# Optimization experiments

Hardware: AMD Instinct MI355X
Metric: run time of the kernel (lower is better)

Reference implementation:

```python
import jax, jax.numpy as jnp
import numpy as np

# Lorentz (hyperboloid) manifold, curvature parameter K: x0 = sqrt(K + ||x_space||^2)
K = 1.0
LN_EPS = 1e-5
PROJ_EPS = 1e-6
L, D, H, B, S, V = 12, 512, 8, 2, 1024, 50257
DH = D // H  # 64 space dims per head


def add_time(space):
    # lift space components onto the hyperboloid
    t = jnp.sqrt(jnp.sum(space * space, axis=-1, keepdims=True) + K)
    return jnp.concatenate([t, space], axis=-1)


def l_project(z):
    # renormalize an ambient vector onto the hyperboloid (Lorentz midpoint / LResNet normalization)
    inner = -jnp.square(z[..., :1]) + jnp.sum(jnp.square(z[..., 1:]), axis=-1, keepdims=True)
    return jnp.sqrt(K) * z / jnp.sqrt(jnp.clip(-inner, PROJ_EPS, None))


def l_layernorm(x, g, b):
    # LayerNorm on the space part, recompute time
    s = x[..., 1:]
    mu = jnp.mean(s, axis=-1, keepdims=True)
    var = jnp.var(s, axis=-1, keepdims=True)
    s = (s - mu) * jax.lax.rsqrt(var + LN_EPS) * g + b
    return add_time(s)


def setup_inputs() -> dict:
    key = jax.random.key(0)
    ks = jax.random.split(key, 12)
    std_in = D ** -0.5
    std_out = (2 * D * L) ** -0.5  # out_proj_std from the torch init
    inp = {}
    inp['text_tokens'] = jax.random.randint(ks[0], (B, S), 0, V)
    inp['embed_table'] = jax.random.normal(ks[1], (V, D - 1), jnp.float32) * 0.02
    inp['Wq'] = jax.random.normal(ks[2], (L, D, D), jnp.float32) * std_in
    inp['bq'] = jnp.zeros((L, D), jnp.float32)
    inp['Wk'] = jax.random.normal(ks[3], (L, D, D), jnp.float32) * std_in
    inp['bk'] = jnp.zeros((L, D), jnp.float32)
    inp['Wv'] = jax.random.normal(ks[4], (L, D, D), jnp.float32) * std_in
    inp['bv'] = jnp.zeros((L, D), jnp.float32)
    inp['Wo'] = jax.random.normal(ks[5], (L, H * (DH + 1), D - 1), jnp.float32) * std_in
    inp['bo'] = jnp.zeros((L, D - 1), jnp.float32)
    inp['ln1_g'] = jnp.ones((L, D - 1), jnp.float32)
    inp['ln1_b'] = jnp.zeros((L, D - 1), jnp.float32)
    inp['ln2_g'] = jnp.ones((L, D - 1), jnp.float32)
    inp['ln2_b'] = jnp.zeros((L, D - 1), jnp.float32)
    inp['Wfc'] = jax.random.normal(ks[6], (L, D, 4 * D - 1), jnp.float32) * std_in
    inp['bfc'] = jnp.zeros((L, 4 * D - 1), jnp.float32)
    inp['Wpr'] = jax.random.normal(ks[7], (L, 4 * D, D - 1), jnp.float32) * std_out
    inp['bpr'] = jnp.zeros((L, D - 1), jnp.float32)
    inp['res_w1'] = jnp.ones((L,), jnp.float32)
    inp['res_w2'] = jnp.ones((L,), jnp.float32)
    inp['Wfin'] = jax.random.normal(ks[8], (D, D - 1), jnp.float32) * std_in
    inp['bfin'] = jnp.zeros((D - 1,), jnp.float32)
    inp['lnf_g'] = jnp.ones((D - 1,), jnp.float32)
    inp['lnf_b'] = jnp.zeros((D - 1,), jnp.float32)
    return inp


def reference(text_tokens, embed_table, Wq, bq, Wk, bk, Wv, bv, Wo, bo, ln1_g, ln1_b,
              ln2_g, ln2_b, Wfc, bfc, Wpr, bpr, res_w1, res_w2, Wfin, bfin, lnf_g, lnf_b):
    b, s = text_tokens.shape
    scale = 1.0 / np.sqrt(DH)
    # LorentzEmbeddings: space-part lookup, time recomputed
    x = add_time(embed_table[text_tokens])  # [B, S, D]
    causal = jnp.tril(jnp.ones((s, s), bool))  # True = attend
    for i in range(L):
        # --- Lorentz multi-head self-attention ---
        lx = l_layernorm(x, ln1_g[i], ln1_b[i])
        q = add_time((lx @ Wq[i] + bq[i]).reshape(b, s, H, DH))  # [B,S,H,DH+1]
        k = add_time((lx @ Wk[i] + bk[i]).reshape(b, s, H, DH))
        v = add_time((lx @ Wv[i] + bv[i]).reshape(b, s, H, DH))
        qm = jnp.concatenate([-q[..., :1], q[..., 1:]], axis=-1)  # apply Minkowski metric
        linner = jnp.einsum('bihd,bjhd->bhij', qm, k)  # Lorentz inner product <q_i, k_j>_L
        scores = (2.0 * K + 2.0 * linner) * scale     # = -d_L^2(q,k)/sqrt(dh)
        scores = jnp.where(causal[None, None], scores, -1e9)
        a = jax.nn.softmax(scores, axis=-1)
        agg = jnp.einsum('bhij,bjhd->bihd', a, v)      # Lorentz centroid numerator
        agg = l_project(agg)                           # normalize back to hyperboloid
        ax = add_time(agg.reshape(b, s, H * (DH + 1)) @ Wo[i] + bo[i])  # heads-concat proj
        x = l_project(x + res_w1[i] * ax)              # LResNet residual 1
        # --- Lorentz MLP ---
        h = l_layernorm(x, ln2_g[i], ln2_b[i])
        h = add_time(h @ Wfc[i] + bfc[i])              # c_fc: D -> 4D ambient
        h = add_time(jax.nn.gelu(h[..., 1:]))          # LorentzActivation (GELU on space)
        h = add_time(h @ Wpr[i] + bpr[i])              # c_proj: 4D -> D ambient
        x = l_project(x + res_w2[i] * h)               # LResNet residual 2
    x = add_time(x @ Wfin + bfin)                      # final_proj
    x = l_layernorm(x, lnf_g, lnf_b)                   # ln_final
    return x
```

## Files before the change

### kernel.cpp

```cpp
#include <hip/hip_runtime.h>
#include <cstdint>

typedef _Float16 f16;
typedef _Float16 f16x8 __attribute__((ext_vector_type(8)));
typedef float f32x4 __attribute__((ext_vector_type(4)));
typedef unsigned int u32;

#define DEV __device__ __forceinline__

DEV void gll16(const void* g, void* l) {
  __builtin_amdgcn_global_load_lds((const __attribute__((address_space(1))) u32*)g,
                                   (__attribute__((address_space(3))) u32*)l, 16, 0, 0);
}

DEV float block_sum(float v, float* red) {
#pragma unroll
  for (int o = 32; o; o >>= 1) v += __shfl_xor(v, o);
  int w = threadIdx.x >> 6;
  __syncthreads();
  if ((threadIdx.x & 63) == 0) red[w] = v;
  __syncthreads();
  return red[0] + red[1] + red[2] + red[3];
}

__global__ void k_trans(const float* __restrict__ W0, f16* __restrict__ BT0, int K, int N, int Kpad,
                        size_t srcStride, size_t dstStride) {
  __shared__ float t[32][33];
  const float* W = W0 + (size_t)blockIdx.z * srcStride;
  f16* BT = BT0 + (size_t)blockIdx.z * dstStride;
  int n0 = blockIdx.x * 32, k0 = blockIdx.y * 32, tx = threadIdx.x, ty = threadIdx.y;
  for (int i = ty; i < 32; i += 8) {
    int k = k0 + i, n = n0 + tx;
    t[i][tx] = (k < K && n < N) ? W[(size_t)k * N + n] : 0.f;
  }
  __syncthreads();
  for (int i = ty; i < 32; i += 8)
    BT[(size_t)(n0 + i) * Kpad + k0 + tx] = (f16)t[tx][i];
}

__global__ void k_trans3(const float* __restrict__ Wq, const float* __restrict__ Wk,
                         const float* __restrict__ Wv, f16* __restrict__ BT) {
  __shared__ float t[32][33];
  const int layer = blockIdx.z / 3, typ = blockIdx.z % 3;
  const float* W = ((typ == 0) ? Wq : (typ == 1) ? Wk : Wv) + (size_t)layer * 262144;
  f16* dst = BT + (size_t)layer * 786432 + (size_t)typ * 262144;
  int n0 = blockIdx.x * 32, k0 = blockIdx.y * 32, tx = threadIdx.x, ty = threadIdx.y;
  for (int i = ty; i < 32; i += 8) t[i][tx] = W[(size_t)(k0 + i) * 512 + n0 + tx];
  __syncthreads();
  for (int i = ty; i < 32; i += 8) dst[(size_t)(n0 + i) * 512 + k0 + tx] = (f16)t[tx][i];
}

template <int BM, int BN, int KZ, int EPI>
__global__ __launch_bounds__((BM == 128) ? 512 : 256)
void k_gemm(const f16* __restrict__ A, const f16* __restrict__ B,
            int lda, int ldb, int klen, int GM,
            float* __restrict__ O1, float* __restrict__ O2,
            float* __restrict__ O3, float* __restrict__ O4, int ldc,
            const float* __restrict__ c0, const float* __restrict__ c1,
            const float* __restrict__ c2, float* __restrict__ ssq,
            f16* __restrict__ H1, f16* __restrict__ H2, f16* __restrict__ H3) {
  constexpr int NW = (BM == 128) ? 8 : 4;
  constexpr int WM = (BM == 128) ? 4 : 2;
  constexpr int FN = BN / ((NW / WM) * 16);
  const int tid = threadIdx.x, wid = tid >> 6, lane = tid & 63;
  const int l15 = lane & 15, l4 = lane >> 4;
  const int wm = wid % WM, wn = wid / WM;
  const int nwg = gridDim.x;
  int lin = blockIdx.x;
  int wg = (lin & 7) * (nwg >> 3) + (lin >> 3);
  int tn = wg / (GM * KZ);
  int rem = wg - tn * (GM * KZ);
  int tm = rem / KZ, tz = rem - (rem / KZ) * KZ;
  const int m0 = tm * BM, n0 = tn * BN, kbeg = tz * klen, ksteps = klen / 64;
  __shared__ __align__(16) char SM[(BM + BN) * 256];
  f32x4 acc[2][FN];
#pragma unroll
  for (int i = 0; i < 2; i++)
#pragma unroll
    for (int j = 0; j < FN; j++) acc[i][j] = (f32x4){0.f, 0.f, 0.f, 0.f};
  const size_t ldab = (size_t)lda * 2, ldbb = (size_t)ldb * 2;
  const int swz = ((lane & 7) ^ (lane >> 3)) * 16;
  const char* Ab = (const char*)A + (size_t)(m0 + (lane >> 3)) * ldab + swz + (size_t)kbeg * 2;
  const char* Bb = (const char*)B + (size_t)(n0 + (lane >> 3)) * ldbb + swz + (size_t)kbeg * 2;
  auto stage = [&](int buf, int ks) {
    char* da = SM + buf * (BM * 128);
    char* db = SM + 2 * BM * 128 + buf * (BN * 128);
    for (int i = wid; i < BM / 8; i += NW)
      gll16(Ab + (size_t)(i * 8) * ldab + (size_t)ks * 128, da + i * 1024);
    for (int i = wid; i < BN / 8; i += NW)
      gll16(Bb + (size_t)(i * 8) * ldbb + (size_t)ks * 128, db + i * 1024);
  };
  stage(0, 0);
  asm volatile("s_waitcnt vmcnt(0)" ::: "memory");
  __builtin_amdgcn_s_barrier();
  __builtin_amdgcn_sched_barrier(0);
  int cur = 0;
  for (int ks = 0; ks < ksteps; ks++) {
    const bool more = (ks + 1 < ksteps);
    if (more) {
      stage(cur ^ 1, ks + 1);
      asm volatile("s_waitcnt vmcnt(4)" ::: "memory");
    } else {
      asm volatile("s_waitcnt vmcnt(0)" ::: "memory");
    }
    __builtin_amdgcn_s_barrier();
    __builtin_amdgcn_sched_barrier(0);
    const f16* sA = (const f16*)(SM + cur * (BM * 128));
    const f16* sB = (const f16*)(SM + 2 * BM * 128 + cur * (BN * 128));
#pragma unroll
    for (int kk = 0; kk < 2; kk++) {
      f16x8 af[2], bf[FN];
#pragma unroll
      for (int i = 0; i < 2; i++) {
        int row = wm * 32 + i * 16 + l15;
        af[i] = *(const f16x8*)(sA + row * 64 + (((kk * 4 + l4) ^ (l15 & 7)) * 8));
      }
#pragma unroll
      for (int j = 0; j < FN; j++) {
        int row = wn * (FN * 16) + j * 16 + l15;
        bf[j] = *(const f16x8*)(sB + row * 64 + (((kk * 4 + l4) ^ (l15 & 7)) * 8));
      }
#pragma unroll
      for (int i = 0; i < 2; i++)
#pragma unroll
        for (int j = 0; j < FN; j++)
          acc[i][j] = __builtin_amdgcn_mfma_f32_16x16x32_f16(af[i], bf[j], acc[i][j], 0, 0, 0);
    }
    __builtin_amdgcn_sched_barrier(0);
    __builtin_amdgcn_s_barrier();
    cur ^= 1;
  }
  if (EPI == 0) {
#pragma unroll
    for (int i = 0; i < 2; i++) {
      int row0 = m0 + wm * 32 + i * 16 + l4 * 4;
#pragma unroll
      for (int j = 0; j < FN; j++) {
        int col = n0 + wn * (FN * 16) + j * 16 + l15;
#pragma unroll
        for (int r = 0; r < 4; r++) O1[(size_t)(row0 + r) * ldc + col] = acc[i][j][r];
      }
    }
  } else if (EPI == 1) {
    const int cb = (n0 >> 6) + wn;
    const int typ = cb >> 3, h = cb & 7;
    const float* bb = (typ == 0) ? c0 : (typ == 1) ? c1 : c2;
    float bj[FN];
#pragma unroll
    for (int j = 0; j < FN; j++) bj[j] = bb[h * 64 + j * 16 + l15];
    const float qs = (typ == 0) ? 0.25f : 1.0f;
#pragma unroll
    for (int i = 0; i < 2; i++) {
#pragma unroll
      for (int r = 0; r < 4; r++) {
        float y[FN], ss = 0.f;
#pragma unroll
        for (int j = 0; j < FN; j++) { y[j] = acc[i][j][r] + bj[j]; ss += y[j] * y[j]; }
        ss += __shfl_xor(ss, 1); ss += __shfl_xor(ss, 2);
        ss += __shfl_xor(ss, 4); ss += __shfl_xor(ss, 8);
        float t = sqrtf(ss + 1.f);
        int row = m0 + wm * 32 + i * 16 + l4 * 4 + r;
        int b = row >> 10, s = row & 1023, bh = b * 8 + h;
        if (typ < 2) {
          f16* dst = typ ? H2 : H1;
          size_t base = ((size_t)bh * 1024 + s) * 88;
#pragma unroll
          for (int j = 0; j < FN; j++) dst[base + j * 16 + l15] = (f16)(qs * y[j]);
          if (l15 == 0) dst[base + 64] = (f16)(qs * t);
        } else {
#pragma unroll
          for (int j = 0; j < FN; j++)
            H3[((size_t)bh * 80 + j * 16 + l15) * 1024 + s] = (f16)y[j];
          if (l15 == 0) H3[((size_t)bh * 80 + 64) * 1024 + s] = (f16)t;
        }
      }
    }
  } else if (EPI == 2) {
#pragma unroll
    for (int i = 0; i < 2; i++) {
#pragma unroll
      for (int r = 0; r < 4; r++) {
        int row = m0 + wm * 32 + i * 16 + l4 * 4 + r;
        float ss = 0.f;
#pragma unroll
        for (int j = 0; j < FN; j++) {
          int col = n0 + wn * (FN * 16) + j * 16 + l15;
          float gg = 0.f;
          if (col < 2047) {
            float yv = acc[i][j][r] + c0[col];
            float cc = yv * yv * yv;
            gg = 0.5f * yv * (1.f + tanhf(0.7978845608f * (yv + 0.044715f * cc)));
          }
          ss += gg * gg;
          H1[(size_t)row * 2048 + col] = (f16)gg;
        }
        ss += __shfl_xor(ss, 1); ss += __shfl_xor(ss, 2);
        ss += __shfl_xor(ss, 4); ss += __shfl_xor(ss, 8);
        if (l15 == 0) atomicAdd(ssq + row, ss);
      }
    }
  } else {
    float* O = (tz == 0) ? O1 : (tz == 1) ? O2 : (tz == 2) ? O3 : O4;
#pragma unroll
    for (int i = 0; i < 2; i++) {
#pragma unroll
      for (int r = 0; r < 4; r++) {
        int row = m0 + wm * 32 + i * 16 + l4 * 4 + r;
        float t = 0.f;
        if (tz == 0) t = sqrtf(ssq[row] + 1.f);
#pragma unroll
        for (int j = 0; j < FN; j++) {
          int col = n0 + wn * (FN * 16) + j * 16 + l15;
          float v = acc[i][j][r];
          if (tz == 0) v += t * ((col < 511) ? c0[col] : 0.f);
          O[(size_t)row * ldc + col] = v;
        }
      }
    }
  }
}

__global__ void k_embed(const int* __restrict__ tok, const float* __restrict__ tbl,
                        const float* __restrict__ g, const float* __restrict__ bsh,
                        float* __restrict__ x, f16* __restrict__ act) {
  __shared__ float red[4];
  const int m = blockIdx.x, tid = threadIdx.x;
  const float* e = tbl + (size_t)tok[m] * 511;
  float e0 = (tid < 511) ? e[tid] : 0.f;
  float e1 = (tid + 256 < 511) ? e[tid + 256] : 0.f;
  float s1 = block_sum(e0 + e1, red);
  float s2 = block_sum(e0 * e0 + e1 * e1, red);
  float t = sqrtf(s2 + 1.f);
  float* xr = x + (size_t)m * 512;
  if (tid == 0) xr[0] = t;
  if (tid < 511) xr[1 + tid] = e0;
  if (tid + 256 < 511) xr[257 + tid] = e1;
  float mu = s1 / 511.f;
  float var = s2 / 511.f - mu * mu;
  float inv = rsqrtf(var + 1e-5f);
  float n0 = (tid < 511) ? (e0 - mu) * inv * g[tid] + bsh[tid] : 0.f;
  float n1 = (tid + 256 < 511) ? (e1 - mu) * inv * g[tid + 256] + bsh[tid + 256] : 0.f;
  float sn = block_sum(n0 * n0 + n1 * n1, red);
  float t2 = sqrtf(sn + 1.f);
  f16* ar = act + (size_t)m * 512;
  if (tid == 0) ar[0] = (f16)t2;
  if (tid < 511) ar[1 + tid] = (f16)n0;
  if (tid + 256 < 511) ar[257 + tid] = (f16)n1;
}

__launch_bounds__(64)
__global__ void k_attn(const f16* __restrict__ qhat, const f16* __restrict__ khat,
                       const f16* __restrict__ vT, f16* __restrict__ ao) {
  __shared__ f16 sP[16 * 88];
  const int lin = blockIdx.x;
  const int wg = (lin & 7) * 128 + (lin >> 3);
  const int bh = wg >> 6, rt = 63 - (wg & 63);
  const int lane = threadIdx.x, l15 = lane & 15, l4 = lane >> 4;
  const f16* qp = qhat + ((size_t)bh * 1024 + rt * 16) * 88;
  const f16* kp = khat + (size_t)bh * 1024 * 88;
  const f16* vp = vT + (size_t)bh * 80 * 1024;
  f16x8 qf0 = *(const f16x8*)(qp + l15 * 88 + l4 * 8);
  f16x8 qf1 = *(const f16x8*)(qp + l15 * 88 + 32 + l4 * 8);
  float qth[4];
#pragma unroll
  for (int r = 0; r < 4; r++) qth[r] = (float)qp[(l4 * 4 + r) * 88 + 64];
  f32x4 acc[5];
#pragma unroll
  for (int i = 0; i < 5; i++) acc[i] = (f32x4){0, 0, 0, 0};
  float mrun[4] = {-3e38f, -3e38f, -3e38f, -3e38f}, lrun[4] = {0, 0, 0, 0};
  const int nt = (rt >> 2) + 1;
  for (int jt = 0; jt < nt; ++jt) {
    const int j0 = jt * 64;
    const bool dt = (jt == nt - 1);
    f32x4 sc[4];
#pragma unroll
    for (int fn = 0; fn < 4; fn++) {
      const f16* kb = kp + (size_t)(j0 + fn * 16 + l15) * 88;
      f16x8 k0v = *(const f16x8*)(kb + l4 * 8);
      f16x8 k1v = *(const f16x8*)(kb + 32 + l4 * 8);
      f32x4 a = (f32x4){0, 0, 0, 0};
      a = __builtin_amdgcn_mfma_f32_16x16x32_f16(qf0, k0v, a, 0, 0, 0);
      a = __builtin_amdgcn_mfma_f32_16x16x32_f16(qf1, k1v, a, 0, 0, 0);
      sc[fn] = a;
    }
    float s[4][4];
#pragma unroll
    for (int fn = 0; fn < 4; fn++) {
      float ktc = (float)kp[(size_t)(j0 + fn * 16 + l15) * 88 + 64];
      int col = j0 + fn * 16 + l15;
#pragma unroll
      for (int r = 0; r < 4; r++) {
        int row = rt * 16 + l4 * 4 + r;
        float v = sc[fn][r] - qth[r] * ktc;
        s[fn][r] = (!dt || col <= row) ? v : -3e38f;
      }
    }
    float mnew[4], al[4], rs[4];
#pragma unroll
    for (int r = 0; r < 4; r++) {
      float t = fmaxf(fmaxf(s[0][r], s[1][r]), fmaxf(s[2][r], s[3][r]));
#pragma unroll
      for (int o = 8; o; o >>= 1) t = fmaxf(t, __shfl_xor(t, o));
      mnew[r] = fmaxf(mrun[r], t);
      al[r] = exp2f((mrun[r] - mnew[r]) * 1.44269504f);
      mrun[r] = mnew[r];
      rs[r] = 0.f;
    }
#pragma unroll
    for (int fn = 0; fn < 4; fn++)
#pragma unroll
      for (int r = 0; r < 4; r++) {
        float p = exp2f((s[fn][r] - mnew[r]) * 1.44269504f);
        rs[r] += p;
        sP[(l4 * 4 + r) * 88 + fn * 16 + l15] = (f16)p;
      }
#pragma unroll
    for (int r = 0; r < 4; r++) {
#pragma unroll
      for (int o = 8; o; o >>= 1) rs[r] += __shfl_xor(rs[r], o);
      lrun[r] = lrun[r] * al[r] + rs[r];
    }
#pragma unroll
    for (int fd = 0; fd < 5; fd++)
#pragma unroll
      for (int r = 0; r < 4; r++) acc[fd][r] *= al[r];
    asm volatile("s_waitcnt lgkmcnt(0)" ::: "memory");
    __builtin_amdgcn_sched_barrier(0);
#pragma unroll
    for (int ks = 0; ks < 2; ks++) {
      f16x8 pf = *(const f16x8*)(sP + l15 * 88 + ks * 32 + l4 * 8);
#pragma unroll
      for (int fd = 0; fd < 5; fd++) {
        f16x8 vf = *(const f16x8*)(vp + (size_t)(fd * 16 + l15) * 1024 + j0 + ks * 32 + l4 * 8);
        acc[fd] = __builtin_amdgcn_mfma_f32_16x16x32_f16(pf, vf, acc[fd], 0, 0, 0);
      }
    }
  }
  const int b = bh >> 3, h = bh & 7;
#pragma unroll
  for (int r = 0; r < 4; r++) {
    float invl = 1.0f / lrun[r];
    float ss = 0.f, ov[4];
#pragma unroll
    for (int fd = 0; fd < 4; fd++) { ov[fd] = acc[fd][r] * invl; ss += ov[fd] * ov[fd]; }
#pragma unroll
    for (int o = 8; o; o >>= 1) ss += __shfl_xor(ss, o);
    float tv = acc[4][r] * invl;
    tv = __shfl(tv, lane & 48);
    float scp = rsqrtf(fmaxf(tv * tv - ss, 1e-6f));
    int row = rt * 16 + l4 * 4 + r;
    size_t rowbase = ((size_t)b * 1024 + row) * 576;
    size_t rb = rowbase + h * 65;
    if (l15 == 0) ao[rb] = (f16)(tv * scp);
#pragma unroll
    for (int fd = 0; fd < 4; fd++) ao[rb + 1 + fd * 16 + l15] = (f16)(ov[fd] * scp);
    for (int c = l15; c < 56; c += 16) ao[rowbase + 520 + c] = (f16)0.f;
  }
}

__global__ void k_resproj(float* __restrict__ x, const float* __restrict__ r1,
                          const float* __restrict__ r2, const float* __restrict__ r3,
                          const float* __restrict__ r4, int np,
                          const float* __restrict__ bias, const float* __restrict__ resw, int li,
                          const float* __restrict__ g, const float* __restrict__ bsh,
                          f16* __restrict__ act, int applyLN, float* __restrict__ ssq) {
  __shared__ float red[4];
  const int m = blockIdx.x, tid = threadIdx.x;
  const size_t rb = (size_t)m * 512;
  float* xr = x + rb;
  const float rw = resw[li];
  if (tid == 0) ssq[m] = 0.f;
  float y0 = 0.f, y1 = 0.f;
  if (tid < 511) {
    y0 = r1[rb + tid];
    if (np == 4) y0 += r2[rb + tid] + r3[rb + tid] + r4[rb + tid];
    y0 += bias[tid];
  }
  if (tid + 256 < 511) {
    y1 = r1[rb + tid + 256];
    if (np == 4) y1 += r2[rb + tid + 256] + r3[rb + tid + 256] + r4[rb + tid + 256];
    y1 += bias[tid + 256];
  }
  float s2 = block_sum(y0 * y0 + y1 * y1, red);
  float tax = sqrtf(s2 + 1.f);
  float xt = xr[0];
  float u0 = (tid < 511) ? xr[1 + tid] + rw * y0 : 0.f;
  float u1 = (tid + 256 < 511) ? xr[257 + tid] + rw * y1 : 0.f;
  float ut = xt + rw * tax;
  float su = block_sum(u0 + u1, red);
  float su2 = block_sum(u0 * u0 + u1 * u1, red);
  float scp = rsqrtf(fmaxf(ut * ut - su2, 1e-6f));
  float nx0 = u0 * scp, nx1 = u1 * scp, nxt = ut * scp;
  if (tid == 0) xr[0] = nxt;
  if (tid < 511) xr[1 + tid] = nx0;
  if (tid + 256 < 511) xr[257 + tid] = nx1;
  f16* ar = act + rb;
  if (applyLN) {
    float mu = su * scp / 511.f;
    float var = su2 * scp * scp / 511.f - mu * mu;
    float inv = rsqrtf(var + 1e-5f);
    float n0 = (tid < 511) ? (nx0 - mu) * inv * g[tid] + bsh[tid] : 0.f;
    float n1 = (tid + 256 < 511) ? (nx1 - mu) * inv * g[tid + 256] + bsh[tid + 256] : 0.f;
    float sn = block_sum(n0 * n0 + n1 * n1, red);
    float t2 = sqrtf(sn + 1.f);
    if (tid == 0) ar[0] = (f16)t2;
    if (tid < 511) ar[1 + tid] = (f16)n0;
    if (tid + 256 < 511) ar[257 + tid] = (f16)n1;
  } else {
    if (tid == 0) ar[0] = (f16)nxt;
    if (tid < 511) ar[1 + tid] = (f16)nx0;
    if (tid + 256 < 511) ar[257 + tid] = (f16)nx1;
  }
}

__global__ void k_final(const float* __restrict__ raw, const float* __restrict__ bias,
                        const float* __restrict__ g, const float* __restrict__ bsh,
                        float* __restrict__ out) {
  __shared__ float red[4];
  const int m = blockIdx.x, tid = threadIdx.x;
  const float* rr = raw + (size_t)m * 512;
  float y0 = (tid < 511) ? rr[tid] + bias[tid] : 0.f;
  float y1 = (tid + 256 < 511) ? rr[tid + 256] + bias[tid + 256] : 0.f;
  float s1 = block_sum(y0 + y1, red);
  float s2 = block_sum(y0 * y0 + y1 * y1, red);
  float mu = s1 / 511.f;
  float var = s2 / 511.f - mu * mu;
  float inv = rsqrtf(var + 1e-5f);
  float n0 = (tid < 511) ? (y0 - mu) * inv * g[tid] + bsh[tid] : 0.f;
  float n1 = (tid + 256 < 511) ? (y1 - mu) * inv * g[tid + 256] + bsh[tid + 256] : 0.f;
  float sn = block_sum(n0 * n0 + n1 * n1, red);
  float t2 = sqrtf(sn + 1.f);
  float* orow = out + (size_t)m * 512;
  if (tid == 0) orow[0] = t2;
  if (tid < 511) orow[1 + tid] = n0;
  if (tid + 256 < 511) orow[257 + tid] = n1;
}

extern "C" void kernel_launch(void* const* d_in, const int* in_sizes, int n_in,
                              void* d_out, int out_size, void* d_ws, size_t ws_size,
                              hipStream_t stream) {
  (void)in_sizes; (void)n_in; (void)out_size; (void)ws_size;
  const int* tok = (const int*)d_in[0];
  const float* etab = (const float*)d_in[1];
  const float* Wq = (const float*)d_in[2];
  const float* bq = (const float*)d_in[3];
  const float* Wk = (const float*)d_in[4];
  const float* bk = (const float*)d_in[5];
  const float* Wv = (const float*)d_in[6];
  const float* bv = (const float*)d_in[7];
  const float* Wo = (const float*)d_in[8];
  const float* bo = (const float*)d_in[9];
  const float* ln1g = (const float*)d_in[10];
  const float* ln1b = (const float*)d_in[11];
  const float* ln2g = (const float*)d_in[12];
  const float* ln2b = (const float*)d_in[13];
  const float* Wfc = (const float*)d_in[14];
  const float* bfc = (const float*)d_in[15];
  const float* Wpr = (const float*)d_in[16];
  const float* bpr = (const float*)d_in[17];
  const float* rw1 = (const float*)d_in[18];
  const float* rw2 = (const float*)d_in[19];
  const float* Wfin = (const float*)d_in[20];
  const float* bfin = (const float*)d_in[21];
  const float* lnfg = (const float*)d_in[22];
  const float* lnfb = (const float*)d_in[23];

  char* wsb = (char*)d_ws;
  size_t off = 0;
  auto alloc = [&](size_t bytes) -> char* {
    char* p = wsb + off;
    off = (off + bytes + 1023) & ~(size_t)1023;
    return p;
  };
  float* x = (float*)alloc(2048ull * 512 * 4);
  f16* actA = (f16*)alloc(2048ull * 512 * 2);
  float* raw1 = (float*)alloc(2048ull * 512 * 4);
  float* raw2 = (float*)alloc(2048ull * 512 * 4);
  float* raw3 = (float*)alloc(2048ull * 512 * 4);
  float* raw4 = (float*)alloc(2048ull * 512 * 4);
  float* ssq = (float*)alloc(2048ull * 4);
  f16* qhat = (f16*)alloc(16ull * 1024 * 88 * 2);
  f16* khat = (f16*)alloc(16ull * 1024 * 88 * 2);
  f16* vT = (f16*)alloc(16ull * 80 * 1024 * 2);
  f16* ao = (f16*)alloc(2048ull * 576 * 2);
  f16* fcact = (f16*)alloc(2048ull * 2048 * 2);
  f16* wqkvT = (f16*)alloc(12ull * 1536 * 512 * 2);
  f16* woT = (f16*)alloc(12ull * 512 * 576 * 2);
  f16* wfcT = (f16*)alloc(12ull * 2048 * 512 * 2);
  f16* wprT = (f16*)alloc(12ull * 512 * 2048 * 2);
  f16* wfinT = (f16*)alloc(512ull * 512 * 2);

  k_trans3<<<dim3(16, 16, 36), dim3(32, 8), 0, stream>>>(Wq, Wk, Wv, wqkvT);
  k_trans<<<dim3(16, 18, 12), dim3(32, 8), 0, stream>>>(Wo, woT, 520, 511, 576,
                                                        520ull * 511, 512ull * 576);
  k_trans<<<dim3(64, 16, 12), dim3(32, 8), 0, stream>>>(Wfc, wfcT, 512, 2047, 512,
                                                        512ull * 2047, 2048ull * 512);
  k_trans<<<dim3(16, 64, 12), dim3(32, 8), 0, stream>>>(Wpr + 511, wprT, 2047, 511, 2048,
                                                        2048ull * 511, 512ull * 2048);
  k_trans<<<dim3(16, 16, 1), dim3(32, 8), 0, stream>>>(Wfin, wfinT, 512, 511, 512, 0, 0);

  k_embed<<<2048, 256, 0, stream>>>(tok, etab, ln1g, ln1b, x, actA);

  for (int li = 0; li < 12; li++) {
    const f16* wqkvT_l = wqkvT + (size_t)li * 1536 * 512;
    const f16* woT_l = woT + (size_t)li * 512 * 576;
    const f16* wfcT_l = wfcT + (size_t)li * 2048 * 512;
    const f16* wprT_l = wprT + (size_t)li * 512 * 2048;
    const float* Wpr_l = Wpr + (size_t)li * 2048 * 511;
    const float* bq_l = bq + (size_t)li * 512;
    const float* bk_l = bk + (size_t)li * 512;
    const float* bv_l = bv + (size_t)li * 512;
    const float* bo_l = bo + (size_t)li * 511;
    const float* bfc_l = bfc + (size_t)li * 2047;
    const float* bpr_l = bpr + (size_t)li * 511;
    const float* ln2g_l = ln2g + (size_t)li * 511;
    const float* ln2b_l = ln2b + (size_t)li * 511;

    k_gemm<128, 128, 1, 1><<<192, 512, 0, stream>>>(
        actA, wqkvT_l, 512, 512, 512, 16, nullptr, nullptr, nullptr, nullptr, 0,
        bq_l, bk_l, bv_l, nullptr, qhat, khat, vT);
    k_attn<<<1024, 64, 0, stream>>>(qhat, khat, vT, ao);
    k_gemm<64, 64, 1, 0><<<256, 256, 0, stream>>>(
        ao, woT_l, 576, 576, 576, 32, raw1, nullptr, nullptr, nullptr, 512,
        nullptr, nullptr, nullptr, nullptr, nullptr, nullptr, nullptr);
    k_resproj<<<2048, 256, 0, stream>>>(x, raw1, raw1, raw1, raw1, 1, bo_l, rw1, li,
                                        ln2g_l, ln2b_l, actA, 1, ssq);
    k_gemm<128, 128, 1, 2><<<256, 512, 0, stream>>>(
        actA, wfcT_l, 512, 512, 512, 16, nullptr, nullptr, nullptr, nullptr, 0,
        bfc_l, nullptr, nullptr, ssq, fcact, nullptr, nullptr);
    k_gemm<64, 64, 4, 3><<<1024, 256, 0, stream>>>(
        fcact, wprT_l, 2048, 2048, 512, 32, raw1, raw2, raw3, raw4, 512,
        Wpr_l, nullptr, nullptr, ssq, nullptr, nullptr, nullptr);
    const float* ng = (li < 11) ? ln1g + (size_t)(li + 1) * 511 : ln1g;
    const float* nb = (li < 11) ? ln1b + (size_t)(li + 1) * 511 : ln1b;
    k_resproj<<<2048, 256, 0, stream>>>(x, raw1, raw2, raw3, raw4, 4, bpr_l, rw2, li,
                                        ng, nb, actA, (li < 11) ? 1 : 0, ssq);
  }

  k_gemm<64, 64, 1, 0><<<256, 256, 0, stream>>>(
      actA, wfinT, 512, 512, 512, 32, raw1, nullptr, nullptr, nullptr, 512,
      nullptr, nullptr, nullptr, nullptr, nullptr, nullptr, nullptr);
  k_final<<<2048, 256, 0, stream>>>(raw1, bfin, lnfg, lnfb, (float*)d_out);
}
```

Baseline: 1.630 ms.

## Fuse residual/LN row kernels into GEMM tails via last-arriver counters; merge prolog kernels

Removes the separate k_resproj and k_final launches. Each GEMM workgroup stores its partial tile with cache-bypassing stores and bumps a per-row-block atomic counter, and the last workgroup for a row block does the split-K reduction, residual projection and LayerNorm for that block. The weight transposes, embedding and counter reset are merged into one prolog launch. This saves launch overhead and a round trip of the row data, but the serial tail now runs on a single workgroup per row block.

```diff
diff --git a/kernel.cpp b/kernel.cpp
--- a/kernel.cpp
+++ b/kernel.cpp
@@ -12,42 +12,135 @@
   __builtin_amdgcn_global_load_lds((const __attribute__((address_space(1))) u32*)g,
                                    (__attribute__((address_space(3))) u32*)l, 16, 0, 0);
 }
-
-DEV float block_sum(float v, float* red) {
+DEV f32x4 ld16c(const void* p) {
+  f32x4 r;
+  asm volatile("global_load_dwordx4 %0, %1, off sc0 sc1" : "=&v"(r) : "v"(p) : "memory");
+  return r;
+}
+DEV float ld4p(const void* p) {
+  float r;
+  asm volatile("global_load_dword %0, %1, off" : "=&v"(r) : "v"(p) : "memory");
+  return r;
+}
+DEV void st4c(void* p, float v) {
+  asm volatile("global_store_dword %0, %1, off sc0 sc1" :: "v"(p), "v"(v) : "memory");
+}
+DEV void vmwait() {
+  asm volatile("s_waitcnt vmcnt(0)" ::: "memory");
+  __builtin_amdgcn_sched_barrier(0);
+}
+DEV u32 inc_rlx(u32* p) { return __hip_atomic_fetch_add(p, 1u, __ATOMIC_RELAXED, __HIP_MEMORY_SCOPE_AGENT); }
+
+DEV float wsum(float v) {
 #pragma unroll
   for (int o = 32; o; o >>= 1) v += __shfl_xor(v, o);
-  int w = threadIdx.x >> 6;
-  __syncthreads();
-  if ((threadIdx.x & 63) == 0) red[w] = v;
-  __syncthreads();
-  return red[0] + red[1] + red[2] + red[3];
-}
-
-__global__ void k_trans(const float* __restrict__ W0, f16* __restrict__ BT0, int K, int N, int Kpad,
-                        size_t srcStride, size_t dstStride) {
-  __shared__ float t[32][33];
-  const float* W = W0 + (size_t)blockIdx.z * srcStride;
-  f16* BT = BT0 + (size_t)blockIdx.z * dstStride;
-  int n0 = blockIdx.x * 32, k0 = blockIdx.y * 32, tx = threadIdx.x, ty = threadIdx.y;
-  for (int i = ty; i < 32; i += 8) {
-    int k = k0 + i, n = n0 + tx;
-    t[i][tx] = (k < K && n < N) ? W[(size_t)k * N + n] : 0.f;
-  }
-  __syncthreads();
-  for (int i = ty; i < 32; i += 8)
-    BT[(size_t)(n0 + i) * Kpad + k0 + tx] = (f16)t[tx][i];
-}
-
-__global__ void k_trans3(const float* __restrict__ Wq, const float* __restrict__ Wk,
-                         const float* __restrict__ Wv, f16* __restrict__ BT) {
-  __shared__ float t[32][33];
-  const int layer = blockIdx.z / 3, typ = blockIdx.z % 3;
-  const float* W = ((typ == 0) ? Wq : (typ == 1) ? Wk : Wv) + (size_t)layer * 262144;
-  f16* dst = BT + (size_t)layer * 786432 + (size_t)typ * 262144;
-  int n0 = blockIdx.x * 32, k0 = blockIdx.y * 32, tx = threadIdx.x, ty = threadIdx.y;
-  for (int i = ty; i < 32; i += 8) t[i][tx] = W[(size_t)(k0 + i) * 512 + n0 + tx];
-  __syncthreads();
-  for (int i = ty; i < 32; i += 8) dst[(size_t)(n0 + i) * 512 + k0 + tx] = (f16)t[tx][i];
+  return v;
+}
+
+template <int NP, int MODE>
+DEV void reduce_tile(int m0, const float* r1, const float* r2, const float* r3, const float* r4,
+                     const float* bias, float rw, const float* g, const float* bsh,
+                     float* x, f16* act, float* outp, float* ssqz, int applyLN) {
+  const int wid = threadIdx.x >> 6, lane = threadIdx.x & 63, cbase = lane * 8;
+  for (int t = 0; t < 16; t++) {
+    const int row = m0 + wid * 16 + t;
+    const size_t rb = (size_t)row * 512 + cbase;
+    f32x4 a0 = ld16c(r1 + rb), a1 = ld16c(r1 + rb + 4);
+    f32x4 b0, b1, c0v, c1v, d0, d1;
+    if (NP == 4) {
+      b0 = ld16c(r2 + rb); b1 = ld16c(r2 + rb + 4);
+      c0v = ld16c(r3 + rb); c1v = ld16c(r3 + rb + 4);
+      d0 = ld16c(r4 + rb); d1 = ld16c(r4 + rb + 4);
+    }
+    float xs[8]; float xt = 0.f;
+    if (MODE == 0) {
+      const float* xrowp = x + (size_t)row * 512;
+#pragma unroll
+      for (int j = 0; j < 8; j++) {
+        int c = cbase + j;
+        xs[j] = (c < 511) ? ld4p(xrowp + 1 + c) : 0.f;
+      }
+      xt = ld4p(xrowp);
+    }
+    vmwait();
+    float y[8];
+#pragma unroll
+    for (int j = 0; j < 4; j++) {
+      y[j] = a0[j]; y[4 + j] = a1[j];
+      if (NP == 4) { y[j] += b0[j] + c0v[j] + d0[j]; y[4 + j] += b1[j] + c1v[j] + d1[j]; }
+    }
+    float lss = 0.f;
+#pragma unroll
+    for (int j = 0; j < 8; j++) {
+      int c = cbase + j;
+      y[j] = (c < 511) ? (y[j] + bias[c]) : 0.f;
+      lss += y[j] * y[j];
+    }
+    float ss = wsum(lss);
+    if (MODE == 1) {
+      float lsu = 0.f;
+#pragma unroll
+      for (int j = 0; j < 8; j++) lsu += y[j];
+      float su = wsum(lsu);
+      float mu = su * (1.f / 511.f);
+      float var = ss * (1.f / 511.f) - mu * mu;
+      float inv = rsqrtf(var + 1e-5f);
+      float n[8], lsn = 0.f;
+#pragma unroll
+      for (int j = 0; j < 8; j++) {
+        int c = cbase + j;
+        n[j] = (c < 511) ? ((y[j] - mu) * inv * g[c] + bsh[c]) : 0.f;
+        lsn += n[j] * n[j];
+      }
+      float t2 = sqrtf(wsum(lsn) + 1.f);
+      float* orow = outp + (size_t)row * 512;
+      if (lane == 0) orow[0] = t2;
+#pragma unroll
+      for (int j = 0; j < 8; j++) { int c = cbase + j; if (c < 511) orow[1 + c] = n[j]; }
+    } else {
+      float tax = sqrtf(ss + 1.f);
+      float u[8], lsu = 0.f, lsu2 = 0.f;
+#pragma unroll
+      for (int j = 0; j < 8; j++) {
+        int c = cbase + j;
+        u[j] = (c < 511) ? (xs[j] + rw * y[j]) : 0.f;
+        lsu += u[j]; lsu2 += u[j] * u[j];
+      }
+      float su = wsum(lsu), su2 = wsum(lsu2);
+      float ut = xt + rw * tax;
+      float scp = rsqrtf(fmaxf(ut * ut - su2, 1e-6f));
+      float nxt = ut * scp;
+      float nx[8];
+#pragma unroll
+      for (int j = 0; j < 8; j++) nx[j] = u[j] * scp;
+      float* xrow = x + (size_t)row * 512;
+      if (lane == 0) xrow[0] = nxt;
+#pragma unroll
+      for (int j = 0; j < 8; j++) { int c = cbase + j; if (c < 511) xrow[1 + c] = nx[j]; }
+      if (NP == 4 && lane == 0) ssqz[row] = 0.f;
+      f16* arow = act + (size_t)row * 512;
+      if (applyLN) {
+        float mu = su * scp * (1.f / 511.f);
+        float var = su2 * scp * scp * (1.f / 511.f) - mu * mu;
+        float inv = rsqrtf(var + 1e-5f);
+        float n[8], lsn = 0.f;
+#pragma unroll
+        for (int j = 0; j < 8; j++) {
+          int c = cbase + j;
+          n[j] = (c < 511) ? ((nx[j] - mu) * inv * g[c] + bsh[c]) : 0.f;
+          lsn += n[j] * n[j];
+        }
+        float t2 = sqrtf(wsum(lsn) + 1.f);
+        if (lane == 0) arow[0] = (f16)t2;
+#pragma unroll
+        for (int j = 0; j < 8; j++) { int c = cbase + j; if (c < 511) arow[1 + c] = (f16)n[j]; }
+      } else {
+        if (lane == 0) arow[0] = (f16)nxt;
+#pragma unroll
+        for (int j = 0; j < 8; j++) { int c = cbase + j; if (c < 511) arow[1 + c] = (f16)nx[j]; }
+      }
+    }
+  }
 }
 
 template <int BM, int BN, int KZ, int EPI>
@@ -58,7 +151,10 @@
             float* __restrict__ O3, float* __restrict__ O4, int ldc,
             const float* __restrict__ c0, const float* __restrict__ c1,
             const float* __restrict__ c2, float* __restrict__ ssq,
-            f16* __restrict__ H1, f16* __restrict__ H2, f16* __restrict__ H3) {
+            f16* __restrict__ H1, f16* __restrict__ H2, f16* __restrict__ H3,
+            float* __restrict__ x, f16* __restrict__ act, float* __restrict__ outp,
+            const float* __restrict__ lng, const float* __restrict__ lnb,
+            const float* __restrict__ rwv, int li, int applyLN, u32* __restrict__ cnt) {
   constexpr int NW = (BM == 128) ? 8 : 4;
   constexpr int WM = (BM == 128) ? 4 : 2;
   constexpr int FN = BN / ((NW / WM) * 16);
@@ -73,6 +169,7 @@
   int tm = rem / KZ, tz = rem - (rem / KZ) * KZ;
   const int m0 = tm * BM, n0 = tn * BN, kbeg = tz * klen, ksteps = klen / 64;
   __shared__ __align__(16) char SM[(BM + BN) * 256];
+  __shared__ int sred;
   f32x4 acc[2][FN];
 #pragma unroll
   for (int i = 0; i < 2; i++)
@@ -130,18 +227,7 @@
     __builtin_amdgcn_s_barrier();
     cur ^= 1;
   }
-  if (EPI == 0) {
-#pragma unroll
-    for (int i = 0; i < 2; i++) {
-      int row0 = m0 + wm * 32 + i * 16 + l4 * 4;
-#pragma unroll
-      for (int j = 0; j < FN; j++) {
-        int col = n0 + wn * (FN * 16) + j * 16 + l15;
-#pragma unroll
-        for (int r = 0; r < 4; r++) O1[(size_t)(row0 + r) * ldc + col] = acc[i][j][r];
-      }
-    }
-  } else if (EPI == 1) {
+  if (EPI == 1) {
     const int cb = (n0 >> 6) + wn;
     const int typ = cb >> 3, h = cb & 7;
     const float* bb = (typ == 0) ? c0 : (typ == 1) ? c1 : c2;
@@ -175,6 +261,7 @@
         }
       }
     }
+    return;
   } else if (EPI == 2) {
 #pragma unroll
     for (int i = 0; i < 2; i++) {
@@ -199,7 +286,8 @@
         if (l15 == 0) atomicAdd(ssq + row, ss);
       }
     }
-  } else {
+    return;
+  } else if (EPI == 3) {
     float* O = (tz == 0) ? O1 : (tz == 1) ? O2 : (tz == 2) ? O3 : O4;
 #pragma unroll
     for (int i = 0; i < 2; i++) {
@@ -213,39 +301,124 @@
           int col = n0 + wn * (FN * 16) + j * 16 + l15;
           float v = acc[i][j][r];
           if (tz == 0) v += t * ((col < 511) ? c0[col] : 0.f);
-          O[(size_t)row * ldc + col] = v;
+          st4c(&O[(size_t)row * ldc + col], v);
         }
       }
     }
-  }
-}
-
-__global__ void k_embed(const int* __restrict__ tok, const float* __restrict__ tbl,
-                        const float* __restrict__ g, const float* __restrict__ bsh,
-                        float* __restrict__ x, f16* __restrict__ act) {
-  __shared__ float red[4];
-  const int m = blockIdx.x, tid = threadIdx.x;
-  const float* e = tbl + (size_t)tok[m] * 511;
-  float e0 = (tid < 511) ? e[tid] : 0.f;
-  float e1 = (tid + 256 < 511) ? e[tid + 256] : 0.f;
-  float s1 = block_sum(e0 + e1, red);
-  float s2 = block_sum(e0 * e0 + e1 * e1, red);
-  float t = sqrtf(s2 + 1.f);
-  float* xr = x + (size_t)m * 512;
-  if (tid == 0) xr[0] = t;
-  if (tid < 511) xr[1 + tid] = e0;
-  if (tid + 256 < 511) xr[257 + tid] = e1;
-  float mu = s1 / 511.f;
-  float var = s2 / 511.f - mu * mu;
-  float inv = rsqrtf(var + 1e-5f);
-  float n0 = (tid < 511) ? (e0 - mu) * inv * g[tid] + bsh[tid] : 0.f;
-  float n1 = (tid + 256 < 511) ? (e1 - mu) * inv * g[tid + 256] + bsh[tid + 256] : 0.f;
-  float sn = block_sum(n0 * n0 + n1 * n1, red);
-  float t2 = sqrtf(sn + 1.f);
-  f16* ar = act + (size_t)m * 512;
-  if (tid == 0) ar[0] = (f16)t2;
-  if (tid < 511) ar[1 + tid] = (f16)n0;
-  if (tid + 256 < 511) ar[257 + tid] = (f16)n1;
+  } else {
+#pragma unroll
+    for (int i = 0; i < 2; i++) {
+      int row0 = m0 + wm * 32 + i * 16 + l4 * 4;
+#pragma unroll
+      for (int j = 0; j < FN; j++) {
+        int col = n0 + wn * (FN * 16) + j * 16 + l15;
+#pragma unroll
+        for (int r = 0; r < 4; r++) st4c(&O1[(size_t)(row0 + r) * ldc + col], acc[i][j][r]);
+      }
+    }
+  }
+  asm volatile("s_waitcnt vmcnt(0)" ::: "memory");
+  __syncthreads();
+  if (tid == 0) {
+    u32 old = inc_rlx(cnt + tm);
+    const u32 C = (EPI == 3) ? 32u : 8u;
+    sred = ((old % C) == C - 1u);
+  }
+  __syncthreads();
+  if (!sred) return;
+  if (EPI == 3)
+    reduce_tile<4, 0>(m0, O1, O2, O3, O4, c1, rwv[li], lng, lnb, x, act, nullptr, ssq, applyLN);
+  else if (EPI == 4)
+    reduce_tile<1, 0>(m0, O1, nullptr, nullptr, nullptr, c0, rwv[li], lng, lnb, x, act,
+                      nullptr, nullptr, 1);
+  else
+    reduce_tile<1, 1>(m0, O1, nullptr, nullptr, nullptr, c0, 0.f, lng, lnb, nullptr, nullptr,
+                      outp, nullptr, 0);
+}
+
+DEV void trans_tile1(const float* W, f16* BT, int K, int N, int ldk, int n0, int k0,
+                     float* shbuf) {
+  float (*tile)[33] = (float(*)[33])shbuf;
+  int tx = threadIdx.x & 31, ty = threadIdx.x >> 5;
+  for (int i = ty; i < 32; i += 8) {
+    int k = k0 + i, n = n0 + tx;
+    tile[i][tx] = (k < K && n < N) ? W[(size_t)k * N + n] : 0.f;
+  }
+  __syncthreads();
+  for (int i = ty; i < 32; i += 8)
+    BT[(size_t)(n0 + i) * ldk + k0 + tx] = (f16)tile[tx][i];
+}
+
+DEV float block_sum1(float v, float* red) {
+#pragma unroll
+  for (int o = 32; o; o >>= 1) v += __shfl_xor(v, o);
+  int w = threadIdx.x >> 6;
+  __syncthreads();
+  if ((threadIdx.x & 63) == 0) red[w] = v;
+  __syncthreads();
+  return red[0] + red[1] + red[2] + red[3];
+}
+
+__global__ __launch_bounds__(256)
+void k_prolog(const float* __restrict__ Wq, const float* __restrict__ Wk,
+              const float* __restrict__ Wv, const float* __restrict__ Wo,
+              const float* __restrict__ Wfc, const float* __restrict__ Wpr,
+              const float* __restrict__ Wfin,
+              f16* __restrict__ wqkvT, f16* __restrict__ woT, f16* __restrict__ wfcT,
+              f16* __restrict__ wprT, f16* __restrict__ wfinT,
+              const int* __restrict__ tok, const float* __restrict__ etab,
+              const float* __restrict__ g, const float* __restrict__ bsh,
+              float* __restrict__ x, f16* __restrict__ act, float* __restrict__ ssq,
+              u32* __restrict__ cnt) {
+  __shared__ float shbuf[32 * 33];
+  const int bid = blockIdx.x, tid = threadIdx.x;
+  if (bid == 0 && tid < 96) cnt[tid] = 0;
+  if (bid < 9216) {
+    int mat = bid >> 8, tile = bid & 255;
+    int layer = mat / 3, typ = mat % 3;
+    const float* W = ((typ == 0) ? Wq : (typ == 1) ? Wk : Wv) + (size_t)layer * 262144;
+    f16* D = wqkvT + (size_t)layer * 786432 + (size_t)typ * 262144;
+    trans_tile1(W, D, 512, 512, 512, (tile & 15) * 32, (tile >> 4) * 32, shbuf);
+  } else if (bid < 12672) {
+    int id = bid - 9216; int l = id / 288, t = id % 288;
+    trans_tile1(Wo + (size_t)l * 265720, woT + (size_t)l * 294912, 520, 511, 576,
+                (t % 16) * 32, (t / 16) * 32, shbuf);
+  } else if (bid < 24960) {
+    int id = bid - 12672; int l = id >> 10, t = id & 1023;
+    trans_tile1(Wfc + (size_t)l * 1048064, wfcT + (size_t)l * 1048576, 512, 2047, 512,
+                (t % 64) * 32, (t / 64) * 32, shbuf);
+  } else if (bid < 37248) {
+    int id = bid - 24960; int l = id >> 10, t = id & 1023;
+    trans_tile1(Wpr + (size_t)l * 1046528 + 511, wprT + (size_t)l * 1048576, 2047, 511, 2048,
+                (t & 15) * 32, (t >> 4) * 32, shbuf);
+  } else if (bid < 37504) {
+    int id = bid - 37248;
+    trans_tile1(Wfin, wfinT, 512, 511, 512, (id & 15) * 32, (id >> 4) * 32, shbuf);
+  } else {
+    float* red = shbuf;
+    const int m = bid - 37504;
+    const float* e = etab + (size_t)tok[m] * 511;
+    float e0 = (tid < 511) ? e[tid] : 0.f;
+    float e1 = (tid + 256 < 511) ? e[tid + 256] : 0.f;
+    float s1 = block_sum1(e0 + e1, red);
+    float s2 = block_sum1(e0 * e0 + e1 * e1, red);
+    float t = sqrtf(s2 + 1.f);
+    float* xr = x + (size_t)m * 512;
+    if (tid == 0) { xr[0] = t; ssq[m] = 0.f; }
+    if (tid < 511) xr[1 + tid] = e0;
+    if (tid + 256 < 511) xr[257 + tid] = e1;
+    float mu = s1 / 511.f;
+    float var = s2 / 511.f - mu * mu;
+    float inv = rsqrtf(var + 1e-5f);
+    float n0 = (tid < 511) ? (e0 - mu) * inv * g[tid] + bsh[tid] : 0.f;
+    float n1 = (tid + 256 < 511) ? (e1 - mu) * inv * g[tid + 256] + bsh[tid + 256] : 0.f;
+    float sn = block_sum1(n0 * n0 + n1 * n1, red);
+    float t2 = sqrtf(sn + 1.f);
+    f16* ar = act + (size_t)m * 512;
+    if (tid == 0) ar[0] = (f16)t2;
+    if (tid < 511) ar[1 + tid] = (f16)n0;
+    if (tid + 256 < 511) ar[257 + tid] = (f16)n1;
+  }
 }
 
 __launch_bounds__(64)
@@ -356,84 +529,6 @@
     for (int fd = 0; fd < 4; fd++) ao[rb + 1 + fd * 16 + l15] = (f16)(ov[fd] * scp);
     for (int c = l15; c < 56; c += 16) ao[rowbase + 520 + c] = (f16)0.f;
   }
-}
-
-__global__ void k_resproj(float* __restrict__ x, const float* __restrict__ r1,
-                          const float* __restrict__ r2, const float* __restrict__ r3,
-                          const float* __restrict__ r4, int np,
-                          const float* __restrict__ bias, const float* __restrict__ resw, int li,
-                          const float* __restrict__ g, const float* __restrict__ bsh,
-                          f16* __restrict__ act, int applyLN, float* __restrict__ ssq) {
-  __shared__ float red[4];
-  const int m = blockIdx.x, tid = threadIdx.x;
-  const size_t rb = (size_t)m * 512;
-  float* xr = x + rb;
-  const float rw = resw[li];
-  if (tid == 0) ssq[m] = 0.f;
-  float y0 = 0.f, y1 = 0.f;
-  if (tid < 511) {
-    y0 = r1[rb + tid];
-    if (np == 4) y0 += r2[rb + tid] + r3[rb + tid] + r4[rb + tid];
-    y0 += bias[tid];
-  }
-  if (tid + 256 < 511) {
-    y1 = r1[rb + tid + 256];
-    if (np == 4) y1 += r2[rb + tid + 256] + r3[rb + tid + 256] + r4[rb + tid + 256];
-    y1 += bias[tid + 256];
-  }
-  float s2 = block_sum(y0 * y0 + y1 * y1, red);
-  float tax = sqrtf(s2 + 1.f);
-  float xt = xr[0];
-  float u0 = (tid < 511) ? xr[1 + tid] + rw * y0 : 0.f;
-  float u1 = (tid + 256 < 511) ? xr[257 + tid] + rw * y1 : 0.f;
-  float ut = xt + rw * tax;
-  float su = block_sum(u0 + u1, red);
-  float su2 = block_sum(u0 * u0 + u1 * u1, red);
-  float scp = rsqrtf(fmaxf(ut * ut - su2, 1e-6f));
-  float nx0 = u0 * scp, nx1 = u1 * scp, nxt = ut * scp;
-  if (tid == 0) xr[0] = nxt;
-  if (tid < 511) xr[1 + tid] = nx0;
-  if (tid + 256 < 511) xr[257 + tid] = nx1;
-  f16* ar = act + rb;
-  if (applyLN) {
-    float mu = su * scp / 511.f;
-    float var = su2 * scp * scp / 511.f - mu * mu;
-    float inv = rsqrtf(var + 1e-5f);
-    float n0 = (tid < 511) ? (nx0 - mu) * inv * g[tid] + bsh[tid] : 0.f;
-    float n1 = (tid + 256 < 511) ? (nx1 - mu) * inv * g[tid + 256] + bsh[tid + 256] : 0.f;
-    float sn = block_sum(n0 * n0 + n1 * n1, red);
-    float t2 = sqrtf(sn + 1.f);
-    if (tid == 0) ar[0] = (f16)t2;
-    if (tid < 511) ar[1 + tid] = (f16)n0;
-    if (tid + 256 < 511) ar[257 + tid] = (f16)n1;
-  } else {
-    if (tid == 0) ar[0] = (f16)nxt;
-    if (tid < 511) ar[1 + tid] = (f16)nx0;
-    if (tid + 256 < 511) ar[257 + tid] = (f16)nx1;
-  }
-}
-
-__global__ void k_final(const float* __restrict__ raw, const float* __restrict__ bias,
-                        const float* __restrict__ g, const float* __restrict__ bsh,
-                        float* __restrict__ out) {
-  __shared__ float red[4];
-  const int m = blockIdx.x, tid = threadIdx.x;
-  const float* rr = raw + (size_t)m * 512;
-  float y0 = (tid < 511) ? rr[tid] + bias[tid] : 0.f;
-  float y1 = (tid + 256 < 511) ? rr[tid + 256] + bias[tid + 256] : 0.f;
-  float s1 = block_sum(y0 + y1, red);
-  float s2 = block_sum(y0 * y0 + y1 * y1, red);
-  float mu = s1 / 511.f;
-  float var = s2 / 511.f - mu * mu;
-  float inv = rsqrtf(var + 1e-5f);
-  float n0 = (tid < 511) ? (y0 - mu) * inv * g[tid] + bsh[tid] : 0.f;
-  float n1 = (tid + 256 < 511) ? (y1 - mu) * inv * g[tid + 256] + bsh[tid + 256] : 0.f;
-  float sn = block_sum(n0 * n0 + n1 * n1, red);
-  float t2 = sqrtf(sn + 1.f);
-  float* orow = out + (size_t)m * 512;
-  if (tid == 0) orow[0] = t2;
-  if (tid < 511) orow[1 + tid] = n0;
-  if (tid + 256 < 511) orow[257 + tid] = n1;
 }
 
 extern "C" void kernel_launch(void* const* d_in, const int* in_sizes, int n_in,
@@ -472,7 +567,7 @@
     off = (off + bytes + 1023) & ~(size_t)1023;
     return p;
   };
-  float* x = (float*)alloc(2048ull * 512 * 4);
+  float* x = (float*)alloc(2048ull * 512 * 4 + 1024);
   f16* actA = (f16*)alloc(2048ull * 512 * 2);
   float* raw1 = (float*)alloc(2048ull * 512 * 4);
   float* raw2 = (float*)alloc(2048ull * 512 * 4);
@@ -489,17 +584,11 @@
   f16* wfcT = (f16*)alloc(12ull * 2048 * 512 * 2);
   f16* wprT = (f16*)alloc(12ull * 512 * 2048 * 2);
   f16* wfinT = (f16*)alloc(512ull * 512 * 2);
-
-  k_trans3<<<dim3(16, 16, 36), dim3(32, 8), 0, stream>>>(Wq, Wk, Wv, wqkvT);
-  k_trans<<<dim3(16, 18, 12), dim3(32, 8), 0, stream>>>(Wo, woT, 520, 511, 576,
-                                                        520ull * 511, 512ull * 576);
-  k_trans<<<dim3(64, 16, 12), dim3(32, 8), 0, stream>>>(Wfc, wfcT, 512, 2047, 512,
-                                                        512ull * 2047, 2048ull * 512);
-  k_trans<<<dim3(16, 64, 12), dim3(32, 8), 0, stream>>>(Wpr + 511, wprT, 2047, 511, 2048,
-                                                        2048ull * 511, 512ull * 2048);
-  k_trans<<<dim3(16, 16, 1), dim3(32, 8), 0, stream>>>(Wfin, wfinT, 512, 511, 512, 0, 0);
-
-  k_embed<<<2048, 256, 0, stream>>>(tok, etab, ln1g, ln1b, x, actA);
+  u32* cnt = (u32*)alloc(512);
+
+  k_prolog<<<39552, 256, 0, stream>>>(Wq, Wk, Wv, Wo, Wfc, Wpr, Wfin,
+                                      wqkvT, woT, wfcT, wprT, wfinT,
+                                      tok, etab, ln1g, ln1b, x, actA, ssq, cnt);
 
   for (int li = 0; li < 12; li++) {
     const f16* wqkvT_l = wqkvT + (size_t)li * 1536 * 512;
@@ -515,30 +604,30 @@
     const float* bpr_l = bpr + (size_t)li * 511;
     const float* ln2g_l = ln2g + (size_t)li * 511;
     const float* ln2b_l = ln2b + (size_t)li * 511;
+    const float* ng = (li < 11) ? ln1g + (size_t)(li + 1) * 511 : ln1g;
+    const float* nb = (li < 11) ? ln1b + (size_t)(li + 1) * 511 : ln1b;
 
     k_gemm<128, 128, 1, 1><<<192, 512, 0, stream>>>(
         actA, wqkvT_l, 512, 512, 512, 16, nullptr, nullptr, nullptr, nullptr, 0,
-        bq_l, bk_l, bv_l, nullptr, qhat, khat, vT);
+        bq_l, bk_l, bv_l, nullptr, qhat, khat, vT,
+        nullptr, nullptr, nullptr, nullptr, nullptr, nullptr, 0, 0, nullptr);
     k_attn<<<1024, 64, 0, stream>>>(qhat, khat, vT, ao);
-    k_gemm<64, 64, 1, 0><<<256, 256, 0, stream>>>(
+    k_gemm<64, 64, 1, 4><<<256, 256, 0, stream>>>(
         ao, woT_l, 576, 576, 576, 32, raw1, nullptr, nullptr, nullptr, 512,
-        nullptr, nullptr, nullptr, nullptr, nullptr, nullptr, nullptr);
-    k_resproj<<<2048, 256, 0, stream>>>(x, raw1, raw1, raw1, raw1, 1, bo_l, rw1, li,
-                                        ln2g_l, ln2b_l, actA, 1, ssq);
+        bo_l, nullptr, nullptr, nullptr, nullptr, nullptr, nullptr,
+        x, actA, nullptr, ln2g_l, ln2b_l, rw1, li, 1, cnt);
     k_gemm<128, 128, 1, 2><<<256, 512, 0, stream>>>(
         actA, wfcT_l, 512, 512, 512, 16, nullptr, nullptr, nullptr, nullptr, 0,
-        bfc_l, nullptr, nullptr, ssq, fcact, nullptr, nullptr);
+        bfc_l, nullptr, nullptr, ssq, fcact, nullptr, nullptr,
+        nullptr, nullptr, nullptr, nullptr, nullptr, nullptr, 0, 0, nullptr);
     k_gemm<64, 64, 4, 3><<<1024, 256, 0, stream>>>(
         fcact, wprT_l, 2048, 2048, 512, 32, raw1, raw2, raw3, raw4, 512,
-        Wpr_l, nullptr, nullptr, ssq, nullptr, nullptr, nullptr);
-    const float* ng = (li < 11) ? ln1g + (size_t)(li + 1) * 511 : ln1g;
-    const float* nb = (li < 11) ? ln1b + (size_t)(li + 1) * 511 : ln1b;
-    k_resproj<<<2048, 256, 0, stream>>>(x, raw1, raw2, raw3, raw4, 4, bpr_l, rw2, li,
-                                        ng, nb, actA, (li < 11) ? 1 : 0, ssq);
-  }
-
-  k_gemm<64, 64, 1, 0><<<256, 256, 0, stream>>>(
+        Wpr_l, bpr_l, nullptr, ssq, nullptr, nullptr, nullptr,
+        x, actA, nullptr, ng, nb, rw2, li, (li < 11) ? 1 : 0, cnt + 32);
+  }
+
+  k_gemm<64, 64, 1, 5><<<256, 256, 0, stream>>>(
       actA, wfinT, 512, 512, 512, 32, raw1, nullptr, nullptr, nullptr, 512,
-      nullptr, nullptr, nullptr, nullptr, nullptr, nullptr, nullptr);
-  k_final<<<2048, 256, 0, stream>>>(raw1, bfin, lnfg, lnfb, (float*)d_out);
-}
+      bfin, nullptr, nullptr, nullptr, nullptr, nullptr, nullptr,
+      nullptr, nullptr, (float*)d_out, lnfg, lnfb, nullptr, 0, 0, cnt + 64);
+}
```

After: 3.771 ms. +131.3%, slower.
